# Optimization experiments

Hardware: AMD Instinct MI355X
Metric: run time of the kernel (lower is better)

Reference implementation:

```python
import jax, jax.numpy as jnp
import numpy as np

N = 500_000          # nodes
E = 8_000_000        # edges (avg degree 16)
C = 2                # in/out channels
STEP_DIM = 8
NUM_STEPS = 100
K = 2                # k_hops -> powers [0, 1]
HID = 8              # hidden_layers


def setup_inputs() -> dict:
    key = jax.random.key(0)
    ks = jax.random.split(key, 6)
    X = jax.random.normal(ks[0], (N, C), dtype=jnp.float32)
    edge_index = jax.random.randint(ks[1], (2, E), 0, N, dtype=jnp.int32)
    step_emb = jax.random.normal(ks[2], (NUM_STEPS, STEP_DIM), dtype=jnp.float32)
    d_in0 = C + STEP_DIM  # 10
    # layer 0: one Linear per power p in {0,1}
    W0 = jax.random.normal(ks[3], (K, d_in0, C), dtype=jnp.float32) / np.sqrt(d_in0).astype(np.float32)
    b0 = jnp.zeros((K, C), dtype=jnp.float32)
    # layers 1..7, stacked for lax.scan
    Wh = jax.random.normal(ks[4], (HID - 1, K, C, C), dtype=jnp.float32) / np.sqrt(C).astype(np.float32)
    bh = jnp.zeros((HID - 1, K, C), dtype=jnp.float32)
    return dict(X=X, edge_index=edge_index, step_index=7, step_emb=step_emb,
                W0=W0, b0=b0, Wh=Wh, bh=bh)


def _make_prop(edge_index, n):
    """GCN-normalized propagation with self-loops (PyG gcn_norm), as used by MixHopConv."""
    src, dst = edge_index[0], edge_index[1]
    # in-degree on destination nodes, +1 for the self-loop
    deg = jnp.zeros((n,), jnp.float32).at[dst].add(1.0) + 1.0
    dis = jax.lax.rsqrt(deg)  # deg^{-1/2}; deg >= 1 so no inf handling needed
    edge_w = dis[src] * dis[dst]  # [E]

    def prop(x):
        msg = x[src] * edge_w[:, None]                      # [E, F] gather
        out = jax.ops.segment_sum(msg, dst, num_segments=n)  # [N, F] scatter-add
        return out + x * (dis * dis)[:, None]               # self-loop term
    return prop


def reference(X, edge_index, step_index, step_emb, W0, b0, Wh, bh):
    n = X.shape[0]
    prop = _make_prop(edge_index, n)

    s = jnp.broadcast_to(step_emb[step_index], (n, STEP_DIM))
    x = jnp.concatenate([X, s], axis=-1)  # [N, 10]

    # layer 0: concat(xW0, (Ax)W1) -> view(-1,K,C).sum(1) -> relu  ==  relu(xW0+b0 + (Ax)W1+b1)
    x = jax.nn.relu(x @ W0[0] + b0[0] + prop(x) @ W0[1] + b0[1])  # [N, 2]

    def body(x, wb):
        W, b = wb  # W: [K, C, C], b: [K, C]
        h = x @ W[0] + b[0] + prop(x) @ W[1] + b[1]
        return jax.nn.relu(h), None

    x, _ = jax.lax.scan(body, x, (Wh, bh))
    return x
```

## Files before the change

kernel.cpp:

```cpp
#include <hip/hip_runtime.h>


constexpr int NN = 500000;
constexpr int NE = 8000000;
constexpr int STEP_DIM = 8;
constexpr int HIDM1 = 7;

constexpr int BSH  = 9;
constexpr int BNOD = 1 << BSH;
constexpr int NBUK = (NN + BNOD - 1) / BNOD;
constexpr int SLOT = 10240;
constexpr int WSLOT = 1280;
constexpr unsigned SENT = (unsigned)BNOD << 19;

constexpr int PA_NBLK = 500;
constexpr int PA_EPB  = NE / PA_NBLK;
constexpr int PA_QPB  = PA_EPB / 4;
constexpr int PA_SC   = NBUK + 1;

typedef unsigned u32x4 __attribute__((ext_vector_type(4)));

__device__ __forceinline__ int swiz(int p) {
  int w = p / WSLOT;
  int r = p - w * WSLOT;
  int tid = r / 20;
  int j = r - tid * 20;
  return w * WSLOT + ((j >> 2) << 8) + (tid << 2) + (j & 3);
}

__device__ __forceinline__ int wave_iscan(int v, int lane) {
#pragma unroll
  for (int off = 1; off < 64; off <<= 1) {
    int n = __shfl_up(v, off, 64);
    if (lane >= off) v += n;
  }
  return v;
}


__global__ __launch_bounds__(512) void k_lsort(const int* __restrict__ src,
                                               const int* __restrict__ dst,
                                               unsigned* __restrict__ colraw,
                                               int* __restrict__ starts2) {
  __shared__ unsigned stage[PA_EPB];
  __shared__ int hist[NBUK];
  __shared__ int tsum[512];
  int b = blockIdx.x, t = threadIdx.x;
  for (int h = t; h < NBUK; h += 512) hist[h] = 0;
  __syncthreads();
  const int4* d4p = (const int4*)dst + (size_t)b * PA_QPB;
  const int4* s4p = (const int4*)src + (size_t)b * PA_QPB;
  for (int i = t; i < PA_QPB; i += 512) {
    int4 d = d4p[i];
    atomicAdd(&hist[d.x >> BSH], 1);
    atomicAdd(&hist[d.y >> BSH], 1);
    atomicAdd(&hist[d.z >> BSH], 1);
    atomicAdd(&hist[d.w >> BSH], 1);
  }
  __syncthreads();
  int h0 = 2 * t, h1 = 2 * t + 1;
  int a0 = (h0 < NBUK) ? hist[h0] : 0;
  int a1 = (h1 < NBUK) ? hist[h1] : 0;
  tsum[t] = a0 + a1;
  __syncthreads();
  for (int o = 1; o < 512; o <<= 1) {
    int v = (t >= o) ? tsum[t - o] : 0;
    __syncthreads();
    tsum[t] += v;
    __syncthreads();
  }
  int ex = tsum[t] - (a0 + a1);
  __syncthreads();
  if (h0 < NBUK) hist[h0] = ex;
  if (h1 < NBUK) hist[h1] = ex + a0;
  __syncthreads();
  int* st = starts2 + (size_t)b * PA_SC;
  for (int h = t; h < NBUK; h += 512) st[h] = hist[h];
  if (t == 0) st[NBUK] = PA_EPB;
  __syncthreads();
  for (int i = t; i < PA_QPB; i += 512) {
    int4 d = d4p[i];
    int4 s = s4p[i];
    int p0 = atomicAdd(&hist[d.x >> BSH], 1);
    stage[p0] = ((unsigned)(d.x & (BNOD - 1)) << 19) | (unsigned)s.x;
    int p1 = atomicAdd(&hist[d.y >> BSH], 1);
    stage[p1] = ((unsigned)(d.y & (BNOD - 1)) << 19) | (unsigned)s.y;
    int p2 = atomicAdd(&hist[d.z >> BSH], 1);
    stage[p2] = ((unsigned)(d.z & (BNOD - 1)) << 19) | (unsigned)s.z;
    int p3 = atomicAdd(&hist[d.w >> BSH], 1);
    stage[p3] = ((unsigned)(d.w & (BNOD - 1)) << 19) | (unsigned)s.w;
  }
  __syncthreads();
  u32x4* out4 = (u32x4*)(colraw + (size_t)b * PA_EPB);
  for (int i = t; i < PA_QPB; i += 512) {
    u32x4 q;
    q[0] = stage[4 * i + 0];
    q[1] = stage[4 * i + 1];
    q[2] = stage[4 * i + 2];
    q[3] = stage[4 * i + 3];
    __builtin_nontemporal_store(q, out4 + i);
  }
}


__global__ __launch_bounds__(512) void k_sortA(const unsigned* __restrict__ colraw,
                                               const int* __restrict__ starts2,
                                               unsigned* __restrict__ col2,
                                               const float2* __restrict__ X,
                                               const float* __restrict__ W0,
                                               const float* __restrict__ step_emb,
                                               const int* __restrict__ step_index,
                                               float* __restrict__ dis,
                                               float2* __restrict__ qtab) {
  __shared__ unsigned stage[SLOT];
  __shared__ int hist[BNOD];
  __shared__ int rp[PA_NBLK + 1];
  __shared__ int rs[PA_NBLK];
  __shared__ int wpart[8];
  int h = blockIdx.x, t = threadIdx.x;
  int wv = t >> 6, lane = t & 63;
  int s = 0, len = 0;
  if (t < PA_NBLK) {
    s = starts2[(size_t)t * PA_SC + h];
    len = starts2[(size_t)t * PA_SC + h + 1] - s;
  }
  hist[t] = 0;
  int incl = wave_iscan(len, lane);
  if (lane == 63) wpart[wv] = incl;
  __syncthreads();
  int wpre = 0, tot = 0;
#pragma unroll
  for (int k = 0; k < 8; ++k) {
    int pv = wpart[k];
    if (k < wv) wpre += pv;
    tot += pv;
  }
  int pos = wpre + incl - len;
  if (t < PA_NBLK) {
    rp[t] = pos;
    rs[t] = s;
  }
  if (t == 511) rp[PA_NBLK] = tot;
  __syncthreads();
  int ns = tot;
  if (ns > SLOT) ns = SLOT;
  {
    int g = t >> 4, gl = t & 15;
    for (int r = g; r < PA_NBLK; r += 32) {
      int P = rp[r];
      int L = rp[r + 1] - P;
      const unsigned* rw = colraw + (size_t)r * PA_EPB + rs[r];
      for (int j = gl; j < L; j += 16) {
        int p = P + j;
        if (p < SLOT) stage[p] = rw[j];
      }
    }
  }
  __syncthreads();
  for (int i = t; i < ns; i += 512)
    atomicAdd(&hist[stage[i] >> 19], 1);
  __syncthreads();
  int deg = hist[t];
  int incl2 = wave_iscan(deg, lane);
  if (lane == 63) wpart[wv] = incl2;
  __syncthreads();
  int wpre2 = 0;
#pragma unroll
  for (int k = 0; k < 8; ++k) {
    if (k < wv) wpre2 += wpart[k];
  }
  hist[t] = wpre2 + incl2 - deg;
  __syncthreads();
  unsigned* base = col2 + (size_t)h * SLOT;
  for (int i = t; i < ns; i += 512) {
    unsigned p = stage[i];
    int posQ = atomicAdd(&hist[(int)(p >> 19)], 1);
    if (posQ < SLOT) base[swiz(posQ)] = p;
  }
  for (int j = ns + t; j < SLOT; j += 512) base[swiz(j)] = SENT;
  int i = (h << BSH) + t;
  if (i < NN) {
    float d = rsqrtf((float)deg + 1.0f);
    dis[i] = d;
    float2 x = X[i];
    const float* sv = step_emb + step_index[0] * STEP_DIM;
    float c1_0 = 0.f, c1_1 = 0.f;
#pragma unroll
    for (int j = 0; j < STEP_DIM; ++j) {
      c1_0 += sv[j] * W0[20 + (2 + j) * 2 + 0];
      c1_1 += sv[j] * W0[20 + (2 + j) * 2 + 1];
    }
    qtab[i] = make_float2(d * (x.x * W0[20] + x.y * W0[22] + c1_0),
                          d * (x.x * W0[21] + x.y * W0[23] + c1_1));
  }
}


__device__ __forceinline__ void load_ebuf(const unsigned* __restrict__ col2,
                                          int b, int w, int l, unsigned* ebuf) {
  const unsigned* bp = col2 + (size_t)b * SLOT + w * WSLOT + l * 4;
#pragma unroll
  for (int g = 0; g < 5; ++g) {
    u32x4 v = *(const u32x4*)(bp + g * 256);
    ebuf[g * 4 + 0] = v[0];
    ebuf[g * 4 + 1] = v[1];
    ebuf[g * 4 + 2] = v[2];
    ebuf[g * 4 + 3] = v[3];
  }
}

__device__ __forceinline__ void gather_acc(const unsigned* ebuf,
                                           const float2* __restrict__ tab,
                                           float* acc) {
  float2 vals[20];
#pragma unroll
  for (int j = 0; j < 20; ++j) vals[j] = tab[ebuf[j] & 0x7FFFF];
  int cur = BNOD;
  float rx = 0.f, ry = 0.f;
#pragma unroll
  for (int j = 0; j < 20; ++j) {
    int ld = (int)(ebuf[j] >> 19);
    if (ld != cur) {
      atomicAdd(&acc[cur * 2 + 0], rx);
      atomicAdd(&acc[cur * 2 + 1], ry);
      cur = ld;
      rx = vals[j].x;
      ry = vals[j].y;
    } else {
      rx += vals[j].x;
      ry += vals[j].y;
    }
  }
  atomicAdd(&acc[cur * 2 + 0], rx);
  atomicAdd(&acc[cur * 2 + 1], ry);
}


__global__ __launch_bounds__(512, 4) void k_blayer0(const unsigned* __restrict__ col2,
                                                    const float2* __restrict__ qtab,
                                                    const float2* __restrict__ X,
                                                    const float* __restrict__ dis,
                                                    const float* __restrict__ W0,
                                                    const float* __restrict__ b0,
                                                    const float* __restrict__ step_emb,
                                                    const int* __restrict__ step_index,
                                                    float2* __restrict__ xs_out) {
  __shared__ float acc[(BNOD + 1) * 2];
  int b = blockIdx.x, t = threadIdx.x;
  for (int j = t; j < (BNOD + 1) * 2; j += 512) acc[j] = 0.f;
  __syncthreads();
  int w = t >> 6, l = t & 63;
  unsigned ebuf[20];
  load_ebuf(col2, b, w, l, ebuf);
  gather_acc(ebuf, qtab, acc);
  __syncthreads();
  const float* sv = step_emb + step_index[0] * STEP_DIM;
  float c00 = b0[0] + b0[2], c01 = b0[1] + b0[3];
#pragma unroll
  for (int j = 0; j < STEP_DIM; ++j) {
    c00 += sv[j] * W0[(2 + j) * 2 + 0];
    c01 += sv[j] * W0[(2 + j) * 2 + 1];
  }
  int i = (b << BSH) + t;
  if (i < NN) {
    float d = dis[i];
    float2 x = X[i];
    float2 qv = qtab[i];
    float h0 = c00 + x.x * W0[0] + x.y * W0[2] + d * (acc[t * 2 + 0] + qv.x);
    float h1 = c01 + x.x * W0[1] + x.y * W0[3] + d * (acc[t * 2 + 1] + qv.y);
    h0 = fmaxf(h0, 0.f);
    h1 = fmaxf(h1, 0.f);
    xs_out[i] = make_float2(d * h0, d * h1);
  }
}

__global__ __launch_bounds__(512, 4) void k_blayer(const unsigned* __restrict__ col2,
                                                   const float* __restrict__ dis,
                                                   const float2* __restrict__ xs_in,
                                                   const float* __restrict__ W,
                                                   const float* __restrict__ bb,
                                                   float2* __restrict__ xs_out,
                                                   float2* __restrict__ out,
                                                   int last) {
  __shared__ float acc[(BNOD + 1) * 2];
  int b = blockIdx.x, t = threadIdx.x;
  for (int j = t; j < (BNOD + 1) * 2; j += 512) acc[j] = 0.f;
  __syncthreads();
  int w = t >> 6, l = t & 63;
  unsigned ebuf[20];
  load_ebuf(col2, b, w, l, ebuf);
  gather_acc(ebuf, xs_in, acc);
  __syncthreads();
  int i = (b << BSH) + t;
  if (i < NN) {
    float d = dis[i];
    float2 xsv = xs_in[i];
    float inv = 1.0f / d;
    float xx = xsv.x * inv, xy = xsv.y * inv;
    float px = d * (acc[t * 2 + 0] + xsv.x);
    float py = d * (acc[t * 2 + 1] + xsv.y);
    float h0 = bb[0] + bb[2] + xx * W[0] + xy * W[2] + px * W[4] + py * W[6];
    float h1 = bb[1] + bb[3] + xx * W[1] + xy * W[3] + px * W[5] + py * W[7];
    h0 = fmaxf(h0, 0.f);
    h1 = fmaxf(h1, 0.f);
    if (last) {
      out[i] = make_float2(h0, h1);
    } else {
      xs_out[i] = make_float2(d * h0, d * h1);
    }
  }
}


extern "C" void kernel_launch(void* const* d_in, const int* in_sizes, int n_in,
                              void* d_out, int out_size, void* d_ws, size_t ws_size,
                              hipStream_t stream) {
  const float2* X        = (const float2*)d_in[0];
  const int*    edge     = (const int*)d_in[1];
  const int*    src      = edge;
  const int*    dstp     = edge + NE;
  const int*    step_idx = (const int*)d_in[2];
  const float*  step_emb = (const float*)d_in[3];
  const float*  W0       = (const float*)d_in[4];
  const float*  b0       = (const float*)d_in[5];
  const float*  Wh       = (const float*)d_in[6];
  const float*  bbias    = (const float*)d_in[7];

  int*      ip      = (int*)d_ws;
  unsigned* col2    = (unsigned*)ip;
  size_t    o       = (size_t)NBUK * SLOT;
  unsigned* colraw  = (unsigned*)(ip + o);  o += NE;
  int*      starts2 = ip + o;               o += ((size_t)PA_NBLK * PA_SC + 8) & ~(size_t)3;
  float*    dis     = (float*)(ip + o);     o += 500224;
  float2*   bufA    = (float2*)(ip + o);    o += 2 * 500224;
  float2*   bufB    = (float2*)(ip + o);

  k_lsort<<<PA_NBLK, 512, 0, stream>>>(src, dstp, colraw, starts2);
  k_sortA<<<NBUK, 512, 0, stream>>>(colraw, starts2, col2, X, W0,
                                    step_emb, step_idx, dis, bufA);

  k_blayer0<<<NBUK, 512, 0, stream>>>(col2, bufA, X, dis, W0, b0,
                                      step_emb, step_idx, bufB);
  float2* cur = bufB;
  float2* nxt = bufA;
  for (int l = 0; l < HIDM1; ++l) {
    k_blayer<<<NBUK, 512, 0, stream>>>(col2, dis, cur, Wh + l * 8,
                                       bbias + l * 4, nxt, (float2*)d_out,
                                       l == HIDM1 - 1 ? 1 : 0);
    float2* tmp = cur;
    cur = nxt;
    nxt = tmp;
  }
}
```

Before: 544.9 us.

## Fuse two-pass bucket sort into single pass with global atomic bucket offsets

Replaces the local-sort-then-per-bucket-regather pipeline with a single sort kernel. Each block claims space in each bucket's slot region through a global atomic and writes the swizzled entries straight into the final edge array, which a new fill kernel pre-populates with sentinels. Node degrees are now counted with global atomics during the histogram pass, and a separate small kernel computes the normalisation factors and the first-layer table. This drops the intermediate edge buffer round trip and the extra gather kernel. The cost is many random global atomics, and entries within a bucket are no longer ordered by destination node, which downstream kernels must tolerate.

```diff
diff --git a/kernel.cpp b/kernel.cpp
--- a/kernel.cpp
+++ b/kernel.cpp
@@ -16,7 +16,9 @@
 constexpr int PA_NBLK = 500;
 constexpr int PA_EPB  = NE / PA_NBLK;
 constexpr int PA_QPB  = PA_EPB / 4;
-constexpr int PA_SC   = NBUK + 1;
+
+constexpr int DEG_PAD = 500224;
+constexpr int GB_PAD  = 1024;
 
 typedef unsigned u32x4 __attribute__((ext_vector_type(4)));
 
@@ -28,22 +30,31 @@
   return w * WSLOT + ((j >> 2) << 8) + (tid << 2) + (j & 3);
 }
 
-__device__ __forceinline__ int wave_iscan(int v, int lane) {
-#pragma unroll
-  for (int off = 1; off < 64; off <<= 1) {
-    int n = __shfl_up(v, off, 64);
-    if (lane >= off) v += n;
-  }
-  return v;
-}
-
-
-__global__ __launch_bounds__(512) void k_lsort(const int* __restrict__ src,
-                                               const int* __restrict__ dst,
-                                               unsigned* __restrict__ colraw,
-                                               int* __restrict__ starts2) {
+
+__global__ __launch_bounds__(256) void k_fill(unsigned* __restrict__ col2,
+                                              int* __restrict__ degz) {
+  int idx = blockIdx.x * 256 + threadIdx.x;
+  int stride = gridDim.x * 256;
+  const int NC4 = (NBUK * SLOT) / 4;
+  u32x4 sv;
+  sv[0] = SENT; sv[1] = SENT; sv[2] = SENT; sv[3] = SENT;
+  u32x4* c4 = (u32x4*)col2;
+  for (int i = idx; i < NC4; i += stride) c4[i] = sv;
+  const int ND4 = (DEG_PAD + GB_PAD) / 4;
+  int4 z = make_int4(0, 0, 0, 0);
+  int4* d4 = (int4*)degz;
+  for (int i = idx; i < ND4; i += stride) d4[i] = z;
+}
+
+
+__global__ __launch_bounds__(512) void k_sort(const int* __restrict__ src,
+                                              const int* __restrict__ dst,
+                                              unsigned* __restrict__ col2,
+                                              int* __restrict__ deg,
+                                              int* __restrict__ gbase) {
   __shared__ unsigned stage[PA_EPB];
   __shared__ int hist[NBUK];
+  __shared__ int st2[NBUK];
   __shared__ int tsum[512];
   int b = blockIdx.x, t = threadIdx.x;
   for (int h = t; h < NBUK; h += 512) hist[h] = 0;
@@ -56,6 +67,10 @@
     atomicAdd(&hist[d.y >> BSH], 1);
     atomicAdd(&hist[d.z >> BSH], 1);
     atomicAdd(&hist[d.w >> BSH], 1);
+    atomicAdd(&deg[d.x], 1);
+    atomicAdd(&deg[d.y], 1);
+    atomicAdd(&deg[d.z], 1);
+    atomicAdd(&deg[d.w], 1);
   }
   __syncthreads();
   int h0 = 2 * t, h1 = 2 * t + 1;
@@ -71,12 +86,8 @@
   }
   int ex = tsum[t] - (a0 + a1);
   __syncthreads();
-  if (h0 < NBUK) hist[h0] = ex;
-  if (h1 < NBUK) hist[h1] = ex + a0;
-  __syncthreads();
-  int* st = starts2 + (size_t)b * PA_SC;
-  for (int h = t; h < NBUK; h += 512) st[h] = hist[h];
-  if (t == 0) st[NBUK] = PA_EPB;
+  if (h0 < NBUK) { hist[h0] = ex;      st2[h0] = ex; }
+  if (h1 < NBUK) { hist[h1] = ex + a0; st2[h1] = ex + a0; }
   __syncthreads();
   for (int i = t; i < PA_QPB; i += 512) {
     int4 d = d4p[i];
@@ -91,108 +102,44 @@
     stage[p3] = ((unsigned)(d.w & (BNOD - 1)) << 19) | (unsigned)s.w;
   }
   __syncthreads();
-  u32x4* out4 = (u32x4*)(colraw + (size_t)b * PA_EPB);
-  for (int i = t; i < PA_QPB; i += 512) {
-    u32x4 q;
-    q[0] = stage[4 * i + 0];
-    q[1] = stage[4 * i + 1];
-    q[2] = stage[4 * i + 2];
-    q[3] = stage[4 * i + 3];
-    __builtin_nontemporal_store(q, out4 + i);
-  }
-}
-
-
-__global__ __launch_bounds__(512) void k_sortA(const unsigned* __restrict__ colraw,
-                                               const int* __restrict__ starts2,
-                                               unsigned* __restrict__ col2,
-                                               const float2* __restrict__ X,
-                                               const float* __restrict__ W0,
-                                               const float* __restrict__ step_emb,
-                                               const int* __restrict__ step_index,
-                                               float* __restrict__ dis,
-                                               float2* __restrict__ qtab) {
-  __shared__ unsigned stage[SLOT];
-  __shared__ int hist[BNOD];
-  __shared__ int rp[PA_NBLK + 1];
-  __shared__ int rs[PA_NBLK];
-  __shared__ int wpart[8];
-  int h = blockIdx.x, t = threadIdx.x;
-  int wv = t >> 6, lane = t & 63;
-  int s = 0, len = 0;
-  if (t < PA_NBLK) {
-    s = starts2[(size_t)t * PA_SC + h];
-    len = starts2[(size_t)t * PA_SC + h + 1] - s;
-  }
-  hist[t] = 0;
-  int incl = wave_iscan(len, lane);
-  if (lane == 63) wpart[wv] = incl;
-  __syncthreads();
-  int wpre = 0, tot = 0;
-#pragma unroll
-  for (int k = 0; k < 8; ++k) {
-    int pv = wpart[k];
-    if (k < wv) wpre += pv;
-    tot += pv;
-  }
-  int pos = wpre + incl - len;
-  if (t < PA_NBLK) {
-    rp[t] = pos;
-    rs[t] = s;
-  }
-  if (t == 511) rp[PA_NBLK] = tot;
-  __syncthreads();
-  int ns = tot;
-  if (ns > SLOT) ns = SLOT;
-  {
-    int g = t >> 4, gl = t & 15;
-    for (int r = g; r < PA_NBLK; r += 32) {
-      int P = rp[r];
-      int L = rp[r + 1] - P;
-      const unsigned* rw = colraw + (size_t)r * PA_EPB + rs[r];
-      for (int j = gl; j < L; j += 16) {
-        int p = P + j;
-        if (p < SLOT) stage[p] = rw[j];
-      }
+  int g = t >> 2, gl = t & 3;
+  int lane = t & 63;
+  for (int bin = g; bin < NBUK; bin += 128) {
+    int st = st2[bin];
+    int cnt = hist[bin] - st;
+    int base = 0;
+    if (gl == 0 && cnt > 0) base = atomicAdd(&gbase[bin], cnt);
+    base = __shfl(base, lane & ~3, 64);
+    unsigned* out = col2 + (size_t)bin * SLOT;
+    for (int k = gl; k < cnt; k += 4) {
+      int p = base + k;
+      if (p < SLOT) out[swiz(p)] = stage[st + k];
     }
   }
-  __syncthreads();
-  for (int i = t; i < ns; i += 512)
-    atomicAdd(&hist[stage[i] >> 19], 1);
-  __syncthreads();
-  int deg = hist[t];
-  int incl2 = wave_iscan(deg, lane);
-  if (lane == 63) wpart[wv] = incl2;
-  __syncthreads();
-  int wpre2 = 0;
-#pragma unroll
-  for (int k = 0; k < 8; ++k) {
-    if (k < wv) wpre2 += wpart[k];
-  }
-  hist[t] = wpre2 + incl2 - deg;
-  __syncthreads();
-  unsigned* base = col2 + (size_t)h * SLOT;
-  for (int i = t; i < ns; i += 512) {
-    unsigned p = stage[i];
-    int posQ = atomicAdd(&hist[(int)(p >> 19)], 1);
-    if (posQ < SLOT) base[swiz(posQ)] = p;
-  }
-  for (int j = ns + t; j < SLOT; j += 512) base[swiz(j)] = SENT;
-  int i = (h << BSH) + t;
-  if (i < NN) {
-    float d = rsqrtf((float)deg + 1.0f);
-    dis[i] = d;
-    float2 x = X[i];
-    const float* sv = step_emb + step_index[0] * STEP_DIM;
-    float c1_0 = 0.f, c1_1 = 0.f;
-#pragma unroll
-    for (int j = 0; j < STEP_DIM; ++j) {
-      c1_0 += sv[j] * W0[20 + (2 + j) * 2 + 0];
-      c1_1 += sv[j] * W0[20 + (2 + j) * 2 + 1];
-    }
-    qtab[i] = make_float2(d * (x.x * W0[20] + x.y * W0[22] + c1_0),
-                          d * (x.x * W0[21] + x.y * W0[23] + c1_1));
-  }
+}
+
+
+__global__ __launch_bounds__(512) void k_qtab(const int* __restrict__ deg,
+                                              const float2* __restrict__ X,
+                                              const float* __restrict__ W0,
+                                              const float* __restrict__ step_emb,
+                                              const int* __restrict__ step_index,
+                                              float* __restrict__ dis,
+                                              float2* __restrict__ qtab) {
+  int i = blockIdx.x * 512 + threadIdx.x;
+  if (i >= NN) return;
+  float d = rsqrtf((float)deg[i] + 1.0f);
+  dis[i] = d;
+  float2 x = X[i];
+  const float* sv = step_emb + step_index[0] * STEP_DIM;
+  float c1_0 = 0.f, c1_1 = 0.f;
+#pragma unroll
+  for (int j = 0; j < STEP_DIM; ++j) {
+    c1_0 += sv[j] * W0[20 + (2 + j) * 2 + 0];
+    c1_1 += sv[j] * W0[20 + (2 + j) * 2 + 1];
+  }
+  qtab[i] = make_float2(d * (x.x * W0[20] + x.y * W0[22] + c1_0),
+                        d * (x.x * W0[21] + x.y * W0[23] + c1_1));
 }
 
 
@@ -326,18 +273,17 @@
   const float*  Wh       = (const float*)d_in[6];
   const float*  bbias    = (const float*)d_in[7];
 
-  int*      ip      = (int*)d_ws;
-  unsigned* col2    = (unsigned*)ip;
-  size_t    o       = (size_t)NBUK * SLOT;
-  unsigned* colraw  = (unsigned*)(ip + o);  o += NE;
-  int*      starts2 = ip + o;               o += ((size_t)PA_NBLK * PA_SC + 8) & ~(size_t)3;
-  float*    dis     = (float*)(ip + o);     o += 500224;
-  float2*   bufA    = (float2*)(ip + o);    o += 2 * 500224;
-  float2*   bufB    = (float2*)(ip + o);
-
-  k_lsort<<<PA_NBLK, 512, 0, stream>>>(src, dstp, colraw, starts2);
-  k_sortA<<<NBUK, 512, 0, stream>>>(colraw, starts2, col2, X, W0,
-                                    step_emb, step_idx, dis, bufA);
+  int*      ip    = (int*)d_ws;
+  unsigned* col2  = (unsigned*)ip;
+  int*      deg   = ip + (size_t)NBUK * SLOT;
+  int*      gbase = deg + DEG_PAD;
+  float*    dis   = (float*)(gbase + GB_PAD);
+  float2*   bufA  = (float2*)(dis + DEG_PAD);
+  float2*   bufB  = bufA + DEG_PAD;
+
+  k_fill<<<2048, 256, 0, stream>>>(col2, deg);
+  k_sort<<<PA_NBLK, 512, 0, stream>>>(src, dstp, col2, deg, gbase);
+  k_qtab<<<NBUK, 512, 0, stream>>>(deg, X, W0, step_emb, step_idx, dis, bufA);
 
   k_blayer0<<<NBUK, 512, 0, stream>>>(col2, bufA, X, dis, W0, b0,
                                       step_emb, step_idx, bufB);
```

After: 1.226 ms. +125.0%, slower.
